# Performance work log

Hardware: AMD Instinct MI355X
Metric: run time of the kernel (lower is better)

The kernel has to match this reference:

```python
import jax, jax.numpy as jnp
import numpy as np

D_IN = 1024
D_OUT = 1024
CTX_LEN = 2048
BATCH = 4
SEQ = 2048


def setup_inputs() -> dict:
    key = jax.random.key(0)
    kx, kq, kk, kv = jax.random.split(key, 4)
    x = jax.random.normal(kx, (BATCH, SEQ, D_IN), dtype=jnp.float32)
    s = 1.0 / np.sqrt(D_IN)
    # torch nn.Linear weight is (d_out, d_in); store transposed for x @ W
    W_q = jax.random.uniform(kq, (D_IN, D_OUT), dtype=jnp.float32, minval=-s, maxval=s)
    W_k = jax.random.uniform(kk, (D_IN, D_OUT), dtype=jnp.float32, minval=-s, maxval=s)
    W_v = jax.random.uniform(kv, (D_IN, D_OUT), dtype=jnp.float32, minval=-s, maxval=s)
    return {"x": x, "W_q": W_q, "W_k": W_k, "W_v": W_v}


def reference(x, W_q, W_k, W_v):
    b, n, _ = x.shape
    d_out = W_q.shape[1]
    q = x @ W_q            # [b, n, d_out]
    k = x @ W_k
    v = x @ W_v
    scores = jnp.einsum('bqd,bkd->bqk', q, k)  # [b, n, n]
    causal = jnp.triu(jnp.ones((n, n), dtype=bool), k=1)
    scores = jnp.where(causal, -jnp.inf, scores)
    attn = jax.nn.softmax(scores / jnp.sqrt(jnp.float32(d_out)), axis=-1)
    # dropout p=0.0 -> identity
    return jnp.einsum('bqk,bkd->bqd', attn, v)
```

## Files before the change

### kernel.cpp

```cpp
#include <hip/hip_runtime.h>
#include <hip/hip_bf16.h>

#define BATCH 4
#define SEQ   2048
#define DIN   1024
#define DOUT  1024
#define N3    3072
#define MTOT  (BATCH*SEQ)

typedef __hip_bfloat16 bf16;
typedef __attribute__((ext_vector_type(8))) short bf16x8;
typedef __attribute__((ext_vector_type(4))) float f32x4;

#define MFMA(a,b,c) __builtin_amdgcn_mfma_f32_16x16x32_bf16(a,b,c,0,0,0)

union pack4 { bf16 h[4]; uint2 u2; };
union pack8 { bf16 h[8]; bf16x8 v; };

__device__ __forceinline__ void gl16(const bf16* g, bf16* l)
{
    __builtin_amdgcn_global_load_lds(
        (const __attribute__((address_space(1))) void*)g,
        (__attribute__((address_space(3))) void*)l, 16, 0, 0);
}


__global__ __launch_bounds__(256)
void k_prep(const float* __restrict__ x, const float* __restrict__ Wq,
            const float* __restrict__ Wk, const float* __restrict__ Wv,
            bf16* __restrict__ xb, bf16* __restrict__ Wt)
{
    __shared__ bf16 t[64][68];
    const int bid = blockIdx.x;
    if (bid < 8192) {
        long i = ((long)bid * 256 + threadIdx.x) * 4;
        float4 v = *(const float4*)(x + i);
        pack4 o;
        o.h[0] = __float2bfloat16(v.x);
        o.h[1] = __float2bfloat16(v.y);
        o.h[2] = __float2bfloat16(v.z);
        o.h[3] = __float2bfloat16(v.w);
        *(uint2*)(xb + i) = o.u2;
        return;
    }
    const int idx = bid - 8192;
    const int mat = idx >> 8;
    const int rem = idx & 255;
    const int k0 = (rem >> 4) * 64, n0 = (rem & 15) * 64;
    const float* W = (mat == 0) ? Wq : ((mat == 1) ? Wk : Wv);
#pragma unroll
    for (int p = 0; p < 4; ++p) {
        int kr = p * 16 + (threadIdx.x >> 4);
        int c4 = (threadIdx.x & 15) * 4;
        float4 v = *(const float4*)&W[(long)(k0 + kr) * DOUT + n0 + c4];
        t[c4 + 0][kr] = __float2bfloat16(v.x);
        t[c4 + 1][kr] = __float2bfloat16(v.y);
        t[c4 + 2][kr] = __float2bfloat16(v.z);
        t[c4 + 3][kr] = __float2bfloat16(v.w);
    }
    __syncthreads();
    bf16* O = Wt + (long)mat * DIN * DOUT;
#pragma unroll
    for (int i = 0; i < 2; ++i) {
        int l = threadIdx.x + i * 256;
        int n = l >> 3, c8 = (l & 7) * 8;
        pack8 o;
#pragma unroll
        for (int j = 0; j < 8; ++j) o.h[j] = t[n][c8 + j];
        *(bf16x8*)&O[(long)(n0 + n) * DIN + k0 + c8] = o.v;
    }
}


__device__ __forceinline__ void gemm_core(
    const bf16* __restrict__ Ab, long lda,
    const bf16* __restrict__ Bb, long ldb,
    int nk, bf16* __restrict__ As, bf16* __restrict__ Bs,
    f32x4 acc[4][4])
{
    const int tid  = threadIdx.x;
    const int lane = tid & 63;
    const int wave = tid >> 6;
    const int wm = (wave >> 1) * 64;
    const int wn = (wave & 1) * 64;
    const int r  = lane & 15;
    const int qd = lane >> 4;

    const int row0 = tid >> 3;
    const int c    = (tid & 7) ^ (row0 & 7);
    const long aoff = (long)row0 * lda + c * 8;
    const long boff = (long)row0 * ldb + c * 8;
    const long astep = 32 * lda, bstep = 32 * ldb;
    bf16* dA = &As[tid * 8];
    bf16* dB = &Bs[tid * 8];

    for (int kk = 0; kk < nk; ++kk) {
        const bf16* A = Ab + kk * 64 + aoff;
        const bf16* B = Bb + kk * 64 + boff;
#pragma unroll
        for (int i = 0; i < 4; ++i) {
            gl16(A + i * astep, dA + i * 2048);
            gl16(B + i * bstep, dB + i * 2048);
        }
        __syncthreads();
#pragma unroll
        for (int ks = 0; ks < 2; ++ks) {
            const int slot = ((ks * 4 + qd) ^ (r & 7)) * 8;
            bf16x8 af[4], bv[4];
#pragma unroll
            for (int mi = 0; mi < 4; ++mi)
                af[mi] = *(const bf16x8*)&As[(wm + mi * 16 + r) * 64 + slot];
#pragma unroll
            for (int ni = 0; ni < 4; ++ni)
                bv[ni] = *(const bf16x8*)&Bs[(wn + ni * 16 + r) * 64 + slot];
#pragma unroll
            for (int mi = 0; mi < 4; ++mi)
#pragma unroll
                for (int ni = 0; ni < 4; ++ni)
                    acc[mi][ni] = MFMA(af[mi], bv[ni], acc[mi][ni]);
        }
        __syncthreads();
    }
}


__global__ __launch_bounds__(256)
void k_gemm_qkv(const bf16* __restrict__ xb, const bf16* __restrict__ Wt,
                bf16* __restrict__ QK, bf16* __restrict__ Vt)
{
    __shared__ __align__(16) bf16 smem[17408];
    bf16* As = smem;
    bf16* Bs = smem + 8192;
    const int m0 = blockIdx.y * 128, n0 = blockIdx.x * 128;
    f32x4 acc[4][4] = {};
    gemm_core(xb + (long)m0 * DIN, DIN, Wt + (long)n0 * DIN, DIN, DIN / 64, As, Bs, acc);

    const int tid = threadIdx.x;
    const int lane = tid & 63, wave = tid >> 6;
    const int wm = (wave >> 1) * 64, wn = (wave & 1) * 64;
    const int r = lane & 15, qd = lane >> 4;

    if (n0 < 2048) {
#pragma unroll
        for (int mi = 0; mi < 4; ++mi)
#pragma unroll
            for (int ni = 0; ni < 4; ++ni)
#pragma unroll
                for (int j = 0; j < 4; ++j) {
                    int row = m0 + wm + mi * 16 + qd * 4 + j;
                    int col = n0 + wn + ni * 16 + r;
                    QK[(long)row * 2048 + col] = __float2bfloat16(acc[mi][ni][j]);
                }
    } else {
        const int ld = 136;
        bf16* T = smem;
#pragma unroll
        for (int mi = 0; mi < 4; ++mi)
#pragma unroll
            for (int ni = 0; ni < 4; ++ni) {
                pack4 p;
#pragma unroll
                for (int j = 0; j < 4; ++j) p.h[j] = __float2bfloat16(acc[mi][ni][j]);
                int d_l = wn + ni * 16 + r;
                int s_l = wm + mi * 16 + qd * 4;
                *(uint2*)&T[d_l * ld + s_l] = p.u2;
            }
        __syncthreads();
        const int n0v = n0 - 2048;
        const int bb = m0 >> 11;
        const int s0 = m0 & 2047;
        bf16* Ob = Vt + (long)bb * DOUT * SEQ + s0;
#pragma unroll
        for (int p = 0; p < 8; ++p) {
            int l = tid + p * 256;
            int d = l >> 4, s8 = (l & 15) * 8;
            bf16x8 vv = *(const bf16x8*)&T[d * ld + s8];
            *(bf16x8*)&Ob[(long)(n0v + d) * SEQ + s8] = vv;
        }
    }
}


__global__ __launch_bounds__(256, 3)
void k_gemm_scores(const bf16* __restrict__ QK, bf16* __restrict__ P,
                   float* __restrict__ rowSum)
{
    const int bid = blockIdx.x;
    const int b = bid & 3;
    int rem = bid >> 2;
    int qt = 15;
    while (rem > qt) { rem -= (qt + 1); --qt; }
    const int kt = rem;

    __shared__ __align__(16) bf16 smem[17408];
    bf16* As = smem;
    bf16* Bs = smem + 8192;
    const bf16* A  = QK + (long)b * SEQ * 2048;
    const bf16* Bt = A + 1024;
    f32x4 acc[4][4] = {};
    gemm_core(A + (long)qt * 128 * 2048, 2048, Bt + (long)kt * 128 * 2048, 2048,
              DIN / 64, As, Bs, acc);

    bf16* Pb = P + (long)b * SEQ * SEQ;
    float* RS = rowSum + b * SEQ;
    const int tid = threadIdx.x;
    const int lane = tid & 63, wave = tid >> 6;
    const int wm = (wave >> 1) * 64, wn = (wave & 1) * 64;
    const int r = lane & 15, qd = lane >> 4;

    const int ld = 136;
    bf16* T = smem;

    float rp[4][4];
#pragma unroll
    for (int mi = 0; mi < 4; ++mi)
#pragma unroll
        for (int j = 0; j < 4; ++j) rp[mi][j] = 0.f;

#pragma unroll
    for (int mi = 0; mi < 4; ++mi)
#pragma unroll
        for (int ni = 0; ni < 4; ++ni)
#pragma unroll
            for (int j = 0; j < 4; ++j) {
                int row_l = wm + mi * 16 + qd * 4 + j;
                int col_l = wn + ni * 16 + r;
                int row = qt * 128 + row_l;
                int col = kt * 128 + col_l;
                float e = (col > row) ? 0.f : __expf(acc[mi][ni][j] * 0.03125f);
                rp[mi][j] += e;
                T[row_l * ld + col_l] = __float2bfloat16(e);
            }
#pragma unroll
    for (int d = 1; d < 16; d <<= 1)
#pragma unroll
        for (int mi = 0; mi < 4; ++mi)
#pragma unroll
            for (int j = 0; j < 4; ++j)
                rp[mi][j] += __shfl_xor(rp[mi][j], d, 64);
    if (r == 0) {
#pragma unroll
        for (int mi = 0; mi < 4; ++mi)
#pragma unroll
            for (int j = 0; j < 4; ++j) {
                int row = qt * 128 + wm + mi * 16 + qd * 4 + j;
                atomicAdd(&RS[row], rp[mi][j]);
            }
    }
    __syncthreads();
#pragma unroll
    for (int p = 0; p < 8; ++p) {
        int l = tid + p * 256;
        int row_l = l >> 4, c8 = (l & 15) * 8;
        bf16x8 vv = *(const bf16x8*)&T[row_l * ld + c8];
        *(bf16x8*)&Pb[(long)(qt * 128 + row_l) * SEQ + kt * 128 + c8] = vv;
    }
}


__global__ __launch_bounds__(256, 3)
void k_gemm_pv(const bf16* __restrict__ P, const bf16* __restrict__ Vt,
               const float* __restrict__ rowSum, float* __restrict__ O)
{
    const int bid = blockIdx.x;
    const int qt = 15 - (bid >> 5);
    const int b  = (bid >> 3) & 3;
    const int nt = bid & 7;
    __shared__ __align__(16) bf16 As[128 * 64];
    __shared__ __align__(16) bf16 Bs[128 * 64];
    const bf16* A  = P + (long)b * SEQ * SEQ + (long)qt * 128 * SEQ;
    const bf16* Bt = Vt + (long)b * DOUT * SEQ;
    const int nk = (qt + 1) * 2;
    f32x4 acc[4][4] = {};
    gemm_core(A, SEQ, Bt + (long)nt * 128 * SEQ, SEQ, nk, As, Bs, acc);

    float* Ob = O + (long)b * SEQ * DOUT;
    const float* RS = rowSum + b * SEQ;
    const int lane = threadIdx.x & 63, wave = threadIdx.x >> 6;
    const int wm = (wave >> 1) * 64, wn = (wave & 1) * 64;
    const int r = lane & 15, qd = lane >> 4;
#pragma unroll
    for (int mi = 0; mi < 4; ++mi)
#pragma unroll
        for (int j = 0; j < 4; ++j) {
            int row = qt * 128 + wm + mi * 16 + qd * 4 + j;
            float inv = 1.0f / RS[row];
#pragma unroll
            for (int ni = 0; ni < 4; ++ni) {
                int col = nt * 128 + wn + ni * 16 + r;
                Ob[(long)row * DOUT + col] = acc[mi][ni][j] * inv;
            }
        }
}


extern "C" void kernel_launch(void* const* d_in, const int* in_sizes, int n_in,
                              void* d_out, int out_size, void* d_ws, size_t ws_size,
                              hipStream_t stream)
{
    const float* x  = (const float*)d_in[0];
    const float* Wq = (const float*)d_in[1];
    const float* Wk = (const float*)d_in[2];
    const float* Wv = (const float*)d_in[3];
    float* out = (float*)d_out;

    char* ws = (char*)d_ws;
    bf16*  xb = (bf16*)(ws);
    bf16*  Wt = (bf16*)(ws + 16777216);
    bf16*  QK = (bf16*)(ws + 23068672);
    bf16*  Vt = (bf16*)(ws + 56623104);
    bf16*  P  = (bf16*)(ws + 73400320);
    float* RS = (float*)(ws + 106954752);

    hipMemsetAsync(RS, 0, BATCH * SEQ * sizeof(float), stream);
    k_prep<<<dim3(8192 + 768), 256, 0, stream>>>(x, Wq, Wk, Wv, xb, Wt);
    k_gemm_qkv<<<dim3(N3 / 128, MTOT / 128), 256, 0, stream>>>(xb, Wt, QK, Vt);
    k_gemm_scores<<<dim3(544), 256, 0, stream>>>(QK, P, RS);
    k_gemm_pv<<<dim3(512), 256, 0, stream>>>(P, Vt, RS, out);
}
```

Measured before the change: 217.0 us.

## Convert scores and PV kernels to persistent blocks with atomic tile queue

Both attention GEMM kernels become persistent: a fixed grid of 768 blocks repeatedly grabs tile indices from a global atomic counter until the work is exhausted. Tiles are still handed out largest-first in PV (qt descending), so dynamic scheduling aims to balance the triangular causal workload and cut the tail of idle CUs. The counters live in the workspace and are zeroed by extending the existing memset. This adds one atomic and one barrier per tile, and 768 blocks may exceed what can be resident at once.

After: 243.4 us. 1.12x slower.

```diff
diff --git a/kernel.cpp b/kernel.cpp
--- a/kernel.cpp
+++ b/kernel.cpp
@@ -183,114 +183,132 @@
 
 __global__ __launch_bounds__(256, 3)
 void k_gemm_scores(const bf16* __restrict__ QK, bf16* __restrict__ P,
-                   float* __restrict__ rowSum)
-{
-    const int bid = blockIdx.x;
-    const int b = bid & 3;
-    int rem = bid >> 2;
-    int qt = 15;
-    while (rem > qt) { rem -= (qt + 1); --qt; }
-    const int kt = rem;
-
+                   float* __restrict__ rowSum, int* __restrict__ cnt)
+{
     __shared__ __align__(16) bf16 smem[17408];
+    __shared__ int s_t;
+    const int tid = threadIdx.x;
     bf16* As = smem;
     bf16* Bs = smem + 8192;
-    const bf16* A  = QK + (long)b * SEQ * 2048;
-    const bf16* Bt = A + 1024;
-    f32x4 acc[4][4] = {};
-    gemm_core(A + (long)qt * 128 * 2048, 2048, Bt + (long)kt * 128 * 2048, 2048,
-              DIN / 64, As, Bs, acc);
-
-    bf16* Pb = P + (long)b * SEQ * SEQ;
-    float* RS = rowSum + b * SEQ;
+
+    for (;;) {
+        if (tid == 0) s_t = atomicAdd(cnt, 1);
+        __syncthreads();
+        const int t = s_t;
+        if (t >= 544) return;
+
+        const int b = t & 3;
+        int rem = t >> 2;
+        int qt = 15;
+        while (rem > qt) { rem -= (qt + 1); --qt; }
+        const int kt = rem;
+
+        const bf16* A  = QK + (long)b * SEQ * 2048;
+        const bf16* Bt = A + 1024;
+        f32x4 acc[4][4] = {};
+        gemm_core(A + (long)qt * 128 * 2048, 2048, Bt + (long)kt * 128 * 2048,
+                  2048, DIN / 64, As, Bs, acc);
+
+        bf16* Pb = P + (long)b * SEQ * SEQ;
+        float* RS = rowSum + b * SEQ;
+        const int lane = tid & 63, wave = tid >> 6;
+        const int wm = (wave >> 1) * 64, wn = (wave & 1) * 64;
+        const int r = lane & 15, qd = lane >> 4;
+
+        const int ld = 136;
+        bf16* T = smem;
+
+        float rp[4][4];
+#pragma unroll
+        for (int mi = 0; mi < 4; ++mi)
+#pragma unroll
+            for (int j = 0; j < 4; ++j) rp[mi][j] = 0.f;
+
+#pragma unroll
+        for (int mi = 0; mi < 4; ++mi)
+#pragma unroll
+            for (int ni = 0; ni < 4; ++ni)
+#pragma unroll
+                for (int j = 0; j < 4; ++j) {
+                    int row_l = wm + mi * 16 + qd * 4 + j;
+                    int col_l = wn + ni * 16 + r;
+                    int row = qt * 128 + row_l;
+                    int col = kt * 128 + col_l;
+                    float e = (col > row) ? 0.f : __expf(acc[mi][ni][j] * 0.03125f);
+                    rp[mi][j] += e;
+                    T[row_l * ld + col_l] = __float2bfloat16(e);
+                }
+#pragma unroll
+        for (int d = 1; d < 16; d <<= 1)
+#pragma unroll
+            for (int mi = 0; mi < 4; ++mi)
+#pragma unroll
+                for (int j = 0; j < 4; ++j)
+                    rp[mi][j] += __shfl_xor(rp[mi][j], d, 64);
+        if (r == 0) {
+#pragma unroll
+            for (int mi = 0; mi < 4; ++mi)
+#pragma unroll
+                for (int j = 0; j < 4; ++j) {
+                    int row = qt * 128 + wm + mi * 16 + qd * 4 + j;
+                    atomicAdd(&RS[row], rp[mi][j]);
+                }
+        }
+        __syncthreads();
+#pragma unroll
+        for (int p = 0; p < 8; ++p) {
+            int l = tid + p * 256;
+            int row_l = l >> 4, c8 = (l & 15) * 8;
+            bf16x8 vv = *(const bf16x8*)&T[row_l * ld + c8];
+            *(bf16x8*)&Pb[(long)(qt * 128 + row_l) * SEQ + kt * 128 + c8] = vv;
+        }
+    }
+}
+
+
+__global__ __launch_bounds__(256, 3)
+void k_gemm_pv(const bf16* __restrict__ P, const bf16* __restrict__ Vt,
+               const float* __restrict__ rowSum, int* __restrict__ cnt,
+               float* __restrict__ O)
+{
+    __shared__ __align__(16) bf16 As[128 * 64];
+    __shared__ __align__(16) bf16 Bs[128 * 64];
+    __shared__ int s_t;
     const int tid = threadIdx.x;
-    const int lane = tid & 63, wave = tid >> 6;
-    const int wm = (wave >> 1) * 64, wn = (wave & 1) * 64;
-    const int r = lane & 15, qd = lane >> 4;
-
-    const int ld = 136;
-    bf16* T = smem;
-
-    float rp[4][4];
-#pragma unroll
-    for (int mi = 0; mi < 4; ++mi)
-#pragma unroll
-        for (int j = 0; j < 4; ++j) rp[mi][j] = 0.f;
-
-#pragma unroll
-    for (int mi = 0; mi < 4; ++mi)
-#pragma unroll
-        for (int ni = 0; ni < 4; ++ni)
-#pragma unroll
-            for (int j = 0; j < 4; ++j) {
-                int row_l = wm + mi * 16 + qd * 4 + j;
-                int col_l = wn + ni * 16 + r;
-                int row = qt * 128 + row_l;
-                int col = kt * 128 + col_l;
-                float e = (col > row) ? 0.f : __expf(acc[mi][ni][j] * 0.03125f);
-                rp[mi][j] += e;
-                T[row_l * ld + col_l] = __float2bfloat16(e);
-            }
-#pragma unroll
-    for (int d = 1; d < 16; d <<= 1)
-#pragma unroll
-        for (int mi = 0; mi < 4; ++mi)
-#pragma unroll
-            for (int j = 0; j < 4; ++j)
-                rp[mi][j] += __shfl_xor(rp[mi][j], d, 64);
-    if (r == 0) {
+
+    for (;;) {
+        if (tid == 0) s_t = atomicAdd(cnt, 1);
+        __syncthreads();
+        const int t = s_t;
+        if (t >= 512) return;
+
+        const int qt = 15 - (t >> 5);
+        const int b  = (t >> 3) & 3;
+        const int nt = t & 7;
+        const bf16* A  = P + (long)b * SEQ * SEQ + (long)qt * 128 * SEQ;
+        const bf16* Bt = Vt + (long)b * DOUT * SEQ;
+        const int nk = (qt + 1) * 2;
+        f32x4 acc[4][4] = {};
+        gemm_core(A, SEQ, Bt + (long)nt * 128 * SEQ, SEQ, nk, As, Bs, acc);
+
+        float* Ob = O + (long)b * SEQ * DOUT;
+        const float* RS = rowSum + b * SEQ;
+        const int lane = tid & 63, wave = tid >> 6;
+        const int wm = (wave >> 1) * 64, wn = (wave & 1) * 64;
+        const int r = lane & 15, qd = lane >> 4;
 #pragma unroll
         for (int mi = 0; mi < 4; ++mi)
 #pragma unroll
             for (int j = 0; j < 4; ++j) {
                 int row = qt * 128 + wm + mi * 16 + qd * 4 + j;
-                atomicAdd(&RS[row], rp[mi][j]);
+                float inv = 1.0f / RS[row];
+#pragma unroll
+                for (int ni = 0; ni < 4; ++ni) {
+                    int col = nt * 128 + wn + ni * 16 + r;
+                    Ob[(long)row * DOUT + col] = acc[mi][ni][j] * inv;
+                }
             }
     }
-    __syncthreads();
-#pragma unroll
-    for (int p = 0; p < 8; ++p) {
-        int l = tid + p * 256;
-        int row_l = l >> 4, c8 = (l & 15) * 8;
-        bf16x8 vv = *(const bf16x8*)&T[row_l * ld + c8];
-        *(bf16x8*)&Pb[(long)(qt * 128 + row_l) * SEQ + kt * 128 + c8] = vv;
-    }
-}
-
-
-__global__ __launch_bounds__(256, 3)
-void k_gemm_pv(const bf16* __restrict__ P, const bf16* __restrict__ Vt,
-               const float* __restrict__ rowSum, float* __restrict__ O)
-{
-    const int bid = blockIdx.x;
-    const int qt = 15 - (bid >> 5);
-    const int b  = (bid >> 3) & 3;
-    const int nt = bid & 7;
-    __shared__ __align__(16) bf16 As[128 * 64];
-    __shared__ __align__(16) bf16 Bs[128 * 64];
-    const bf16* A  = P + (long)b * SEQ * SEQ + (long)qt * 128 * SEQ;
-    const bf16* Bt = Vt + (long)b * DOUT * SEQ;
-    const int nk = (qt + 1) * 2;
-    f32x4 acc[4][4] = {};
-    gemm_core(A, SEQ, Bt + (long)nt * 128 * SEQ, SEQ, nk, As, Bs, acc);
-
-    float* Ob = O + (long)b * SEQ * DOUT;
-    const float* RS = rowSum + b * SEQ;
-    const int lane = threadIdx.x & 63, wave = threadIdx.x >> 6;
-    const int wm = (wave >> 1) * 64, wn = (wave & 1) * 64;
-    const int r = lane & 15, qd = lane >> 4;
-#pragma unroll
-    for (int mi = 0; mi < 4; ++mi)
-#pragma unroll
-        for (int j = 0; j < 4; ++j) {
-            int row = qt * 128 + wm + mi * 16 + qd * 4 + j;
-            float inv = 1.0f / RS[row];
-#pragma unroll
-            for (int ni = 0; ni < 4; ++ni) {
-                int col = nt * 128 + wn + ni * 16 + r;
-                Ob[(long)row * DOUT + col] = acc[mi][ni][j] * inv;
-            }
-        }
 }
 
 
@@ -311,10 +329,12 @@
     bf16*  Vt = (bf16*)(ws + 56623104);
     bf16*  P  = (bf16*)(ws + 73400320);
     float* RS = (float*)(ws + 106954752);
-
-    hipMemsetAsync(RS, 0, BATCH * SEQ * sizeof(float), stream);
+    int* cntS = (int*)(ws + 106987520);
+    int* cntP = cntS + 1;
+
+    hipMemsetAsync(RS, 0, BATCH * SEQ * sizeof(float) + 128, stream);
     k_prep<<<dim3(8192 + 768), 256, 0, stream>>>(x, Wq, Wk, Wv, xb, Wt);
     k_gemm_qkv<<<dim3(N3 / 128, MTOT / 128), 256, 0, stream>>>(xb, Wt, QK, Vt);
-    k_gemm_scores<<<dim3(544), 256, 0, stream>>>(QK, P, RS);
-    k_gemm_pv<<<dim3(512), 256, 0, stream>>>(P, Vt, RS, out);
-}
+    k_gemm_scores<<<dim3(768), 256, 0, stream>>>(QK, P, RS, cntS);
+    k_gemm_pv<<<dim3(768), 256, 0, stream>>>(P, Vt, RS, cntP, out);
+}
```
